# Optimization experiments

Measured on AMD Instinct MI355X. Metric: run time of the kernel, lower is better.

## Reference

```python
import jax, jax.numpy as jnp
import numpy as np

N = 32           # signal length (samples)
K_TOTAL = 4      # number of pulses (K=[4], single pulse type)
T = 1.0          # sampling period
RESOLUTION = 64
KNOTS = N * RESOLUTION + 1  # 2049 knots per pulse type
BATCH = 256


def setup_inputs() -> dict:
    key = jax.random.key(0)
    k1, k2 = jax.random.split(key)
    # estimated pulse locations, in [0, 1) (remainder maps everything into [0, N))
    t_k_hat = jax.random.uniform(k1, (BATCH, K_TOTAL), dtype=jnp.float32)
    # c_ReLU: second-difference spline coefficients (uniform init in the module)
    c_relu = jax.random.uniform(k2, (KNOTS,), minval=-0.01, maxval=0.01,
                                dtype=jnp.float32)
    # shift = b_ReLU = -t_phi grid (knot locations), non-trainable in the module
    shift = -(jnp.arange(KNOTS, dtype=jnp.float32) / RESOLUTION)
    # init = phi[0] = 0 for the zero/uniform phi initialisation
    init_val = jnp.zeros((1,), dtype=jnp.float32)
    return {"t_k_hat": t_k_hat, "c_relu": c_relu, "shift": shift,
            "init_val": init_val}


def reference(t_k_hat, c_relu, shift, init_val):
    # fc1 = remainder(t_k/T - n, N), shape [B, K, N] -> [B, N, K]
    n_vec = jnp.arange(N, dtype=t_k_hat.dtype)
    fc1 = jnp.remainder(t_k_hat[..., None] / T - n_vec, N)
    fc1 = jnp.swapaxes(fc1, -1, -2)                      # [B, N, K]
    # train_decoder=True constraint: c[-1] = -sum(c[:-1]) (applied functionally)
    head = c_relu[:-1]
    c_eff = jnp.concatenate([head, -jnp.sum(head, keepdims=True)])
    # Block-diagonal Linear(K_total, knots_tot) with all-ones blocks + shift bias
    # followed by block-diagonal c_ReLU contraction == grouped small matvec:
    # phi_hat[b,n,p] = sum_j relu(fc1[b,n,p] + shift[j]) * c_eff[j] + init
    act = jax.nn.relu(fc1[..., None] + shift)            # [B, N, K, knots]
    phi_hat = jnp.einsum('bnkj,j->bnk', act, c_eff) + init_val
    return phi_hat
```

## Files before the change

### kernel.cpp

```cpp
#include <hip/hip_runtime.h>
#include <hip/hip_bf16.h>

#define NN 32
#define K_TOTAL 4
#define RESOLUTION 64
#define KNOTS (NN * RESOLUTION + 1)
#define BATCH 256
#define HEAD 2048
#define OUT_TOTAL (BATCH * NN * K_TOTAL)

__global__ __launch_bounds__(256) void scan_kernel(const float* __restrict__ c_relu,
                                                   double* __restrict__ P) {
    __shared__ double s1[256];
    __shared__ double s2[256];
    const int t = threadIdx.x;
    const int base = t * 8;

    float c[8];
#pragma unroll
    for (int i = 0; i < 8; ++i) c[i] = c_relu[base + i];

    double pre1[8], pre2[8];
    double l1 = 0.0, l2 = 0.0;
#pragma unroll
    for (int i = 0; i < 8; ++i) {
        pre1[i] = l1;
        pre2[i] = l2;
        l1 += (double)c[i];
        l2 += (double)(base + i) * (double)c[i];
    }
    s1[t] = l1;
    s2[t] = l2;

    for (int off = 1; off < 256; off <<= 1) {
        __syncthreads();
        double a1 = 0.0, a2 = 0.0;
        if (t >= off) { a1 = s1[t - off]; a2 = s2[t - off]; }
        __syncthreads();
        if (t >= off) { s1[t] += a1; s2[t] += a2; }
    }
    __syncthreads();

    const double off1 = (t == 0) ? 0.0 : s1[t - 1];
    const double off2 = (t == 0) ? 0.0 : s2[t - 1];

    double* __restrict__ P1 = P;
    double* __restrict__ P2 = P + KNOTS;
#pragma unroll
    for (int i = 0; i < 8; ++i) {
        P1[base + i] = off1 + pre1[i];
        P2[base + i] = off2 + pre2[i];
    }
    if (t == 255) {
        P1[HEAD] = s1[255];
        P2[HEAD] = s2[255];
    }
}

__global__ __launch_bounds__(256) void eval_kernel(const float* __restrict__ t_k,
                                                   const float* __restrict__ init_val,
                                                   const double* __restrict__ P,
                                                   float* __restrict__ out) {
    const int o = blockIdx.x * blockDim.x + threadIdx.x;
    const int k = o & (K_TOTAL - 1);
    const int n = (o >> 2) & (NN - 1);
    const int b = o >> 7;

    const float t = t_k[(b << 2) | k];
    float r = t - (float)n;
    if (r < 0.0f) r += 32.0f;

    const double d = (double)r * 64.0;
    int m = (int)d;
    if ((double)m < d) ++m;
    if (m > HEAD) m = HEAD;

    const double* __restrict__ P1 = P;
    const double* __restrict__ P2 = P + KNOTS;
    const double phi = (double)r * P1[m] - P2[m] * 0.015625 + (double)init_val[0];
    out[o] = (float)phi;
}

extern "C" void kernel_launch(void* const* d_in, const int* in_sizes, int n_in,
                              void* d_out, int out_size, void* d_ws, size_t ws_size,
                              hipStream_t stream) {
    const float* t_k_hat  = (const float*)d_in[0];
    const float* c_relu   = (const float*)d_in[1];
    const float* init_val = (const float*)d_in[3];
    float* out = (float*)d_out;
    double* P = (double*)d_ws;

    scan_kernel<<<1, 256, 0, stream>>>(c_relu, P);
    eval_kernel<<<OUT_TOTAL / 256, 256, 0, stream>>>(t_k_hat, init_val, P, out);
}
```

Before: 63.09 us.

## Fuse prefix-scan and evaluation into one kernel with per-block float scan

```diff
diff --git a/kernel.cpp b/kernel.cpp
--- a/kernel.cpp
+++ b/kernel.cpp
@@ -9,76 +9,72 @@
 #define HEAD 2048
 #define OUT_TOTAL (BATCH * NN * K_TOTAL)
 
-__global__ __launch_bounds__(256) void scan_kernel(const float* __restrict__ c_relu,
-                                                   double* __restrict__ P) {
-    __shared__ double s1[256];
-    __shared__ double s2[256];
+__global__ __launch_bounds__(256) void fused_kernel(const float* __restrict__ t_k,
+                                                    const float* __restrict__ c_relu,
+                                                    const float* __restrict__ init_val,
+                                                    float* __restrict__ out) {
+    __shared__ float P1[KNOTS];
+    __shared__ float P2[KNOTS];
+    __shared__ float tot1[256];
+    __shared__ float tot2[256];
+
     const int t = threadIdx.x;
     const int base = t * 8;
 
-    float c[8];
-#pragma unroll
-    for (int i = 0; i < 8; ++i) c[i] = c_relu[base + i];
+    const float4* __restrict__ c4 = (const float4*)c_relu;
+    const float4 ca = c4[2 * t];
+    const float4 cb = c4[2 * t + 1];
+    float c[8] = {ca.x, ca.y, ca.z, ca.w, cb.x, cb.y, cb.z, cb.w};
 
-    double pre1[8], pre2[8];
-    double l1 = 0.0, l2 = 0.0;
+    float pre1[8], pre2[8];
+    float l1 = 0.0f, l2 = 0.0f;
 #pragma unroll
     for (int i = 0; i < 8; ++i) {
         pre1[i] = l1;
         pre2[i] = l2;
-        l1 += (double)c[i];
-        l2 += (double)(base + i) * (double)c[i];
+        l1 += c[i];
+        l2 += (float)(base + i) * c[i];
     }
-    s1[t] = l1;
-    s2[t] = l2;
+    tot1[t] = l1;
+    tot2[t] = l2;
 
     for (int off = 1; off < 256; off <<= 1) {
         __syncthreads();
-        double a1 = 0.0, a2 = 0.0;
-        if (t >= off) { a1 = s1[t - off]; a2 = s2[t - off]; }
+        float a1 = 0.0f, a2 = 0.0f;
+        if (t >= off) { a1 = tot1[t - off]; a2 = tot2[t - off]; }
         __syncthreads();
-        if (t >= off) { s1[t] += a1; s2[t] += a2; }
+        if (t >= off) { tot1[t] += a1; tot2[t] += a2; }
     }
     __syncthreads();
 
-    const double off1 = (t == 0) ? 0.0 : s1[t - 1];
-    const double off2 = (t == 0) ? 0.0 : s2[t - 1];
-
-    double* __restrict__ P1 = P;
-    double* __restrict__ P2 = P + KNOTS;
+    const float off1 = (t == 0) ? 0.0f : tot1[t - 1];
+    const float off2 = (t == 0) ? 0.0f : tot2[t - 1];
 #pragma unroll
     for (int i = 0; i < 8; ++i) {
         P1[base + i] = off1 + pre1[i];
         P2[base + i] = off2 + pre2[i];
     }
     if (t == 255) {
-        P1[HEAD] = s1[255];
-        P2[HEAD] = s2[255];
+        P1[HEAD] = tot1[255];
+        P2[HEAD] = tot2[255];
     }
-}
+    __syncthreads();
 
-__global__ __launch_bounds__(256) void eval_kernel(const float* __restrict__ t_k,
-                                                   const float* __restrict__ init_val,
-                                                   const double* __restrict__ P,
-                                                   float* __restrict__ out) {
-    const int o = blockIdx.x * blockDim.x + threadIdx.x;
+    const int o = blockIdx.x * 256 + t;
     const int k = o & (K_TOTAL - 1);
     const int n = (o >> 2) & (NN - 1);
     const int b = o >> 7;
 
-    const float t = t_k[(b << 2) | k];
-    float r = t - (float)n;
+    const float tv = t_k[(b << 2) | k];
+    float r = tv - (float)n;
     if (r < 0.0f) r += 32.0f;
 
-    const double d = (double)r * 64.0;
+    const float d = r * 64.0f;
     int m = (int)d;
-    if ((double)m < d) ++m;
+    if ((float)m < d) ++m;
     if (m > HEAD) m = HEAD;
 
-    const double* __restrict__ P1 = P;
-    const double* __restrict__ P2 = P + KNOTS;
-    const double phi = (double)r * P1[m] - P2[m] * 0.015625 + (double)init_val[0];
-    out[o] = (float)phi;
+    out[o] = r * P1[m] - P2[m] * 0.015625f + init_val[0];
 }
 
 extern "C" void kernel_launch(void* const* d_in, const int* in_sizes, int n_in,
@@ -88,8 +84,6 @@
     const float* c_relu   = (const float*)d_in[1];
     const float* init_val = (const float*)d_in[3];
     float* out = (float*)d_out;
-    double* P = (double*)d_ws;
 
-    scan_kernel<<<1, 256, 0, stream>>>(c_relu, P);
-    eval_kernel<<<OUT_TOTAL / 256, 256, 0, stream>>>(t_k_hat, init_val, P, out);
+    fused_kernel<<<OUT_TOTAL / 256, 256, 0, stream>>>(t_k_hat, c_relu, init_val, out);
 }
```

Measured after the change: 60.33 us. -4.4%, faster.
